# Optimization experiments

Hardware: AMD Instinct MI355X
Metric: run time of the kernel (lower is better)

Reference implementation:

```python
import jax, jax.numpy as jnp
import numpy as np

N, E, D, H = 100000, 200000, 384, 768
BN_EPS = 1e-5


def setup_inputs() -> dict:
    key = jax.random.key(0)
    ks = jax.random.split(key, 8)
    w = lambda k, sh: jax.random.normal(k, sh, jnp.float32) * 0.02
    return {
        "x": jax.random.normal(ks[0], (N, D), jnp.float32),
        "edge_attr": jax.random.normal(ks[1], (E, D), jnp.float32),
        "gamma": jnp.ones((D,), jnp.float32),
        "beta": jnp.zeros((D,), jnp.float32),
        "eps": jnp.zeros((), jnp.float32),          # GINE train_eps, init 0
        "W_edge": w(ks[2], (D, D)),
        "b_edge": jnp.zeros((D,), jnp.float32),
        "W1": w(ks[3], (D, H)),
        "b1": jnp.zeros((H,), jnp.float32),
        "W2": w(ks[4], (H, D)),
        "b2": jnp.zeros((D,), jnp.float32),
        "edge_index": jax.random.randint(ks[5], (2, E), 0, N, jnp.int32),
    }


def reference(x, edge_attr, gamma, beta, eps, W_edge, b_edge, W1, b1, W2, b2, edge_index):
    # BatchNorm1d over the node (batch) dimension, training statistics
    mu = jnp.mean(x, axis=0)
    var = jnp.var(x, axis=0)
    h = (x - mu) * jax.lax.rsqrt(var + BN_EPS) * gamma + beta  # [N, D]

    src, dst = edge_index[0], edge_index[1]  # j -> i (PyG source_to_target)
    # GINEConv message: relu(x_j + lin(edge_attr))
    msg = jax.nn.relu(h[src] + edge_attr @ W_edge + b_edge)     # [E, D]
    agg = jax.ops.segment_sum(msg, dst, num_segments=N)         # sum aggregation

    # nn((1+eps)*x_i + agg) where nn = Linear->GELU->Linear
    z = (1.0 + eps) * h + agg
    z = jax.nn.gelu(z @ W1 + b1, approximate=False) @ W2 + b2

    # residual + outer GELU activation (drop_path/dropout = identity at eval)
    return x + jax.nn.gelu(z, approximate=False)
```

## Files before the change

### kernel.cpp

```cpp
#include <hip/hip_runtime.h>
#include <hip/hip_bf16.h>

#define Df 384
#define Hf 768
#define SCAN_CH 4096

typedef __bf16 bf16x8 __attribute__((ext_vector_type(8)));
typedef float f32x4 __attribute__((ext_vector_type(4)));

struct __attribute__((aligned(4))) U12 { unsigned int x, y, z; };

__device__ inline unsigned short f2bf(float f) {
    __hip_bfloat16 h = __float2bfloat16(f);
    return __builtin_bit_cast(unsigned short, h);
}
__device__ inline float bf2f(unsigned short u) {
    unsigned int v = ((unsigned int)u) << 16;
    return __builtin_bit_cast(float, v);
}
__device__ inline float lobf(unsigned int v) { return bf2f((unsigned short)(v & 0xffff)); }
__device__ inline float hibf(unsigned int v) { return bf2f((unsigned short)(v >> 16)); }
__device__ inline unsigned int pk2(float a, float b) {
    return (unsigned int)f2bf(a) | ((unsigned int)f2bf(b) << 16);
}
__device__ inline float gelu_(float v) {
    return 0.5f * v * (1.0f + erff(v * 0.70710678118654752f));
}
__device__ inline void gload16(const void* g, void* l) {
    __builtin_amdgcn_global_load_lds(
        (const __attribute__((address_space(1))) unsigned int*)g,
        (__attribute__((address_space(3))) unsigned int*)l, 16, 0, 0);
}

__global__ void bn_stats(const float* __restrict__ x, float* __restrict__ stats, int N) {
    int t = threadIdx.x;
    int c4 = (t % 96) * 4;
    int rs = t / 96;
    float s0 = 0, s1 = 0, s2 = 0, s3 = 0, q0 = 0, q1 = 0, q2 = 0, q3 = 0;
    for (int r = blockIdx.x * 2 + rs; r < N; r += gridDim.x * 2) {
        float4 v = *(const float4*)(x + (size_t)r * Df + c4);
        s0 += v.x; s1 += v.y; s2 += v.z; s3 += v.w;
        q0 += v.x * v.x; q1 += v.y * v.y; q2 += v.z * v.z; q3 += v.w * v.w;
    }
    unsafeAtomicAdd(&stats[c4 + 0], s0);
    unsafeAtomicAdd(&stats[c4 + 1], s1);
    unsafeAtomicAdd(&stats[c4 + 2], s2);
    unsafeAtomicAdd(&stats[c4 + 3], s3);
    unsafeAtomicAdd(&stats[Df + c4 + 0], q0);
    unsafeAtomicAdd(&stats[Df + c4 + 1], q1);
    unsafeAtomicAdd(&stats[Df + c4 + 2], q2);
    unsafeAtomicAdd(&stats[Df + c4 + 3], q3);
}

__global__ void bn_finalize(const float* __restrict__ stats,
                            const float* __restrict__ gamma,
                            const float* __restrict__ beta,
                            float* __restrict__ coef, int N) {
    int c = threadIdx.x;
    float invN = 1.0f / (float)N;
    float mu = stats[c] * invN;
    float var = stats[Df + c] * invN - mu * mu;
    float rs = rsqrtf(var + 1e-5f);
    float a = gamma[c] * rs;
    coef[c] = a;
    coef[Df + c] = beta[c] - mu * a;
}

__global__ void h_kernel(const float* __restrict__ x, const float* __restrict__ coef,
                         unsigned short* __restrict__ hb, int tot8) {
    int i = blockIdx.x * 256 + threadIdx.x;
    if (i >= tot8) return;
    size_t base = (size_t)i * 8;
    int c = (int)(base % Df);
    float4 x0 = *(const float4*)(x + base);
    float4 x1 = *(const float4*)(x + base + 4);
    const float* a = coef + c;
    const float* b = coef + Df + c;
    uint4 o;
    o.x = pk2(x0.x * a[0] + b[0], x0.y * a[1] + b[1]);
    o.y = pk2(x0.z * a[2] + b[2], x0.w * a[3] + b[3]);
    o.z = pk2(x1.x * a[4] + b[4], x1.y * a[5] + b[5]);
    o.w = pk2(x1.z * a[6] + b[6], x1.w * a[7] + b[7]);
    *(uint4*)(hb + base) = o;
}

__global__ void wtrans3(const float* __restrict__ We, const float* __restrict__ W1,
                        const float* __restrict__ W2,
                        unsigned short* __restrict__ WeT, unsigned short* __restrict__ W1T,
                        unsigned short* __restrict__ W2T) {
    int idx = blockIdx.x * 256 + threadIdx.x;
    if (idx < Df * Df) {
        int k = idx / Df, n = idx % Df;
        WeT[n * Df + k] = f2bf(We[idx]);
    } else if (idx < Df * Df + Df * Hf) {
        int i = idx - Df * Df;
        int k = i / Hf, n = i % Hf;
        W1T[(size_t)n * Df + k] = f2bf(W1[i]);
    } else if (idx < Df * Df + 2 * Df * Hf) {
        int i = idx - (Df * Df + Df * Hf);
        int k = i / Df, n = i % Df;
        W2T[(size_t)n * Hf + k] = f2bf(W2[i]);
    }
}

__global__ void degree_k(const int* __restrict__ dst, int* __restrict__ deg, int E) {
    int e = blockIdx.x * 256 + threadIdx.x;
    if (e < E) atomicAdd(&deg[dst[e]], 1);
}

__global__ void scan1(const int* __restrict__ deg, int* __restrict__ off,
                      int* __restrict__ sums, int N) {
    __shared__ int ts[256];
    int t = threadIdx.x;
    int base = blockIdx.x * SCAN_CH + t * 16;
    int v[16];
    int s = 0;
    for (int j = 0; j < 16; j++) {
        int idx = base + j;
        int d = (idx < N) ? deg[idx] : 0;
        v[j] = s;
        s += d;
    }
    ts[t] = s;
    __syncthreads();
    for (int o = 1; o < 256; o <<= 1) {
        int add = (t >= o) ? ts[t - o] : 0;
        __syncthreads();
        ts[t] += add;
        __syncthreads();
    }
    int pre = t ? ts[t - 1] : 0;
    for (int j = 0; j < 16; j++) {
        int idx = base + j;
        if (idx < N) off[idx] = pre + v[j];
    }
    if (t == 255) sums[blockIdx.x] = ts[255];
}

__global__ void scan2(int* __restrict__ sums, int nb) {
    int acc = 0;
    for (int b = 0; b < nb; b++) { int v = sums[b]; sums[b] = acc; acc += v; }
    sums[nb] = acc;
}

__global__ void scan3(int* __restrict__ off, const int* __restrict__ sums, int N, int nb) {
    int idx = blockIdx.x * 256 + threadIdx.x;
    if (idx < N) off[idx] += sums[idx / SCAN_CH];
    else if (idx == N) off[N] = sums[nb];
}

__global__ void fill_k(const int* __restrict__ dst, const int* __restrict__ src,
                       int* __restrict__ cursor, int* __restrict__ srcp,
                       int* __restrict__ pose, int E) {
    int e = blockIdx.x * 256 + threadIdx.x;
    if (e >= E) return;
    int pos = atomicAdd(&cursor[dst[e]], 1);
    srcp[pos] = src[e];
    pose[e] = pos;
}

__global__ __launch_bounds__(256) void aggregate(
    const unsigned short* __restrict__ msgl, const unsigned short* __restrict__ hb,
    const int* __restrict__ off, const int* __restrict__ srcp,
    const float* __restrict__ epsp,
    unsigned short* __restrict__ zb, int N) {
    int lane = threadIdx.x & 63;
    int wid = threadIdx.x >> 6;
    int nwaves = gridDim.x * 4;
    float s1p = 1.0f + epsp[0];
    int loff = lane * 6;
    for (int i = blockIdx.x * 4 + wid; i < N; i += nwaves) {
        int o0 = off[i], o1 = off[i + 1];
        float a0 = 0, a1 = 0, a2 = 0, a3 = 0, a4 = 0, a5 = 0;
        for (int p = o0; p < o1; ++p) {
            int s = srcp[p];
            U12 mv = *(const U12*)(msgl + (size_t)p * Df + loff);
            U12 hv = *(const U12*)(hb + (size_t)s * Df + loff);
            a0 += fmaxf(lobf(mv.x) + lobf(hv.x), 0.f);
            a1 += fmaxf(hibf(mv.x) + hibf(hv.x), 0.f);
            a2 += fmaxf(lobf(mv.y) + lobf(hv.y), 0.f);
            a3 += fmaxf(hibf(mv.y) + hibf(hv.y), 0.f);
            a4 += fmaxf(lobf(mv.z) + lobf(hv.z), 0.f);
            a5 += fmaxf(hibf(mv.z) + hibf(hv.z), 0.f);
        }
        U12 hv = *(const U12*)(hb + (size_t)i * Df + loff);
        U12 o;
        o.x = pk2(s1p * lobf(hv.x) + a0, s1p * hibf(hv.x) + a1);
        o.y = pk2(s1p * lobf(hv.y) + a2, s1p * hibf(hv.y) + a3);
        o.z = pk2(s1p * lobf(hv.z) + a4, s1p * hibf(hv.z) + a5);
        *(U12*)(zb + (size_t)i * Df + loff) = o;
    }
}

__global__ __launch_bounds__(256, 3) void gemm_ts(
    const unsigned short* __restrict__ Ab,
    const unsigned short* __restrict__ Bt,
    const float* __restrict__ bias,
    unsigned short* __restrict__ outb,
    int M) {
    __shared__ __align__(16) unsigned short Bs[64 * Df];

    const int t = threadIdx.x;
    const int lane = t & 63;
    const int wid = t >> 6;
    const int fr = lane & 15;
    const int kg = lane >> 4;
    const int orig = blockIdx.x;
    const int xcd = orig & 7;
    const int local = orig >> 3;
    const int cs = local % 12;
    const int rsub = local / 12;
    const int cb = cs * 64;
    const int first = xcd * 8 + rsub;
    const int STRIPS = (M + 127) >> 7;

#pragma unroll
    for (int s = 0; s < 12; s++) {
        int u = s * 256 + t;
        int col = u / 48;
        int pos = u - col * 48;
        gload16(Bt + (size_t)(cb + col) * Df + ((pos ^ (col & 7)) << 3),
                &Bs[(s * 256 + wid * 64) * 8]);
    }
    asm volatile("s_waitcnt vmcnt(0)" ::: "memory");
    __builtin_amdgcn_s_barrier();

    float bv[4];
#pragma unroll
    for (int j = 0; j < 4; j++) bv[j] = bias[cb + j * 16 + fr];

    for (int s = first; s < STRIPS; s += 64) {
        const int r0 = s * 128 + wid * 32;
        int ra0 = r0 + fr;       if (ra0 >= M) ra0 = M - 1;
        int ra1 = r0 + 16 + fr;  if (ra1 >= M) ra1 = M - 1;
        const unsigned short* pA0 = Ab + (size_t)ra0 * Df + kg * 8;
        const unsigned short* pA1 = Ab + (size_t)ra1 * Df + kg * 8;

        f32x4 acc[2][4];
#pragma unroll
        for (int i = 0; i < 2; i++)
#pragma unroll
            for (int j = 0; j < 4; j++) acc[i][j] = (f32x4){0.f, 0.f, 0.f, 0.f};

        uint4 a0 = *(const uint4*)(pA0);
        uint4 a1 = *(const uint4*)(pA1);
#pragma unroll
        for (int kt = 0; kt < 12; kt++) {
            uint4 n0, n1;
            if (kt < 11) {
                n0 = *(const uint4*)(pA0 + (kt + 1) * 32);
                n1 = *(const uint4*)(pA1 + (kt + 1) * 32);
            } else { n0 = a0; n1 = a1; }
            bf16x8 bf[4];
#pragma unroll
            for (int j = 0; j < 4; j++) {
                const int cl = j * 16 + fr;
                const int unit = (kt * 4 + kg) ^ (cl & 7);
                bf[j] = *(const bf16x8*)&Bs[(cl * 48 + unit) * 8];
            }
            bf16x8 av0 = __builtin_bit_cast(bf16x8, a0);
            bf16x8 av1 = __builtin_bit_cast(bf16x8, a1);
#pragma unroll
            for (int j = 0; j < 4; j++) {
                acc[0][j] = __builtin_amdgcn_mfma_f32_16x16x32_bf16(av0, bf[j], acc[0][j], 0, 0, 0);
                acc[1][j] = __builtin_amdgcn_mfma_f32_16x16x32_bf16(av1, bf[j], acc[1][j], 0, 0, 0);
            }
            a0 = n0; a1 = n1;
        }

        const int kg4 = kg * 4;
#pragma unroll
        for (int i = 0; i < 2; i++) {
            const int rb = r0 + i * 16 + kg4;
#pragma unroll
            for (int r = 0; r < 4; r++) {
                const int row = rb + r;
                if (row < M) {
#pragma unroll
                    for (int j = 0; j < 4; j++) {
                        outb[(size_t)row * Hf + cb + j * 16 + fr] =
                            f2bf(gelu_(acc[i][j][r] + bv[j]));
                    }
                }
            }
        }
    }
}

template <int EPI, bool ABF16>
__global__ __launch_bounds__(256) void gemm_fused(
    const void* __restrict__ Ap, const unsigned short* __restrict__ Bt,
    const float* __restrict__ bias, int M, int K, int ncols,
    const int* __restrict__ pose,
    unsigned short* __restrict__ outb,
    const float* __restrict__ xres, float* __restrict__ outf, int ldo) {
    __shared__ __align__(16) unsigned short As[2][128 * 32];
    __shared__ __align__(16) unsigned short Bs[2][128 * 32];
    const int t = threadIdx.x;
    const int nwg = gridDim.x;
    const int orig = blockIdx.x;
    const int xcd = orig & 7;
    const int q = nwg >> 3, r = nwg & 7;
    const int wgid = (xcd < r ? xcd * (q + 1) : r * (q + 1) + (xcd - r) * q) + (orig >> 3);
    const int pp = wgid / ncols;
    const int m0 = pp * 128;
    const int n0 = (wgid - pp * ncols) * 128;

    const int lane = t & 63;
    const int wid = t >> 6;
    const int wr = (wid >> 1) << 6;
    const int wc = (wid & 1) << 6;
    const int fr = lane & 15;
    const int kg = lane >> 4;
    const int crow = lane >> 2;
    const int cseg = lane & 3;
    const int sr = t >> 1;
    const int sh = (t & 1) << 4;

    f32x4 acc[4][4];
#pragma unroll
    for (int i = 0; i < 4; i++)
#pragma unroll
        for (int j = 0; j < 4; j++) acc[i][j] = (f32x4){0.f, 0.f, 0.f, 0.f};

    const bool arok = (m0 + sr) < M;
    const size_t arowoff = (size_t)(m0 + sr) * K;
    const int NT = K >> 5;

    auto stageB = [&](int buf, int k0) {
#pragma unroll
        for (int h = 0; h < 2; h++) {
            const int rbase = wid * 32 + h * 16;
            gload16(Bt + (size_t)(n0 + rbase + crow) * K + k0 + cseg * 8,
                    &Bs[buf][rbase * 32]);
        }
    };
    auto stageA16 = [&](int buf, int k0) {
        const unsigned short* Ab = (const unsigned short*)Ap;
#pragma unroll
        for (int h = 0; h < 2; h++) {
            const int rbase = wid * 32 + h * 16;
            if (m0 + rbase + crow < M)
                gload16(Ab + (size_t)(m0 + rbase + crow) * K + k0 + cseg * 8,
                        &As[buf][rbase * 32]);
        }
    };

    if (ABF16) {
        stageA16(0, 0);
    } else if (arok) {
        const float4* p = (const float4*)((const float*)Ap + arowoff + sh);
        float4 f0 = p[0], f1 = p[1], f2 = p[2], f3 = p[3];
        uint4 w0, w1;
        w0.x = pk2(f0.x, f0.y); w0.y = pk2(f0.z, f0.w);
        w0.z = pk2(f1.x, f1.y); w0.w = pk2(f1.z, f1.w);
        w1.x = pk2(f2.x, f2.y); w1.y = pk2(f2.z, f2.w);
        w1.z = pk2(f3.x, f3.y); w1.w = pk2(f3.z, f3.w);
        *(uint4*)&As[0][sr * 32 + sh] = w0;
        *(uint4*)&As[0][sr * 32 + sh + 8] = w1;
    }
    stageB(0, 0);
    __syncthreads();

    int cur = 0;
    for (int kt = 0; kt < NT; ++kt) {
        const int nxt = cur ^ 1;
        const bool more = (kt + 1) < NT;
        float4 f0, f1, f2, f3;
        if (more) {
            const int k0n = (kt + 1) * 32;
            if (ABF16) {
                stageA16(nxt, k0n);
            } else if (arok) {
                const float4* p = (const float4*)((const float*)Ap + arowoff + k0n + sh);
                f0 = p[0]; f1 = p[1]; f2 = p[2]; f3 = p[3];
            }
            stageB(nxt, k0n);
        }

        bf16x8 a[4], b[4];
#pragma unroll
        for (int i = 0; i < 4; i++) a[i] = *(const bf16x8*)&As[cur][(wr + i * 16 + fr) * 32 + kg * 8];
#pragma unroll
        for (int j = 0; j < 4; j++) b[j] = *(const bf16x8*)&Bs[cur][(wc + j * 16 + fr) * 32 + kg * 8];
#pragma unroll
        for (int i = 0; i < 4; i++)
#pragma unroll
            for (int j = 0; j < 4; j++)
                acc[i][j] = __builtin_amdgcn_mfma_f32_16x16x32_bf16(a[i], b[j], acc[i][j], 0, 0, 0);

        if (!ABF16 && more && arok) {
            uint4 w0, w1;
            w0.x = pk2(f0.x, f0.y); w0.y = pk2(f0.z, f0.w);
            w0.z = pk2(f1.x, f1.y); w0.w = pk2(f1.z, f1.w);
            w1.x = pk2(f2.x, f2.y); w1.y = pk2(f2.z, f2.w);
            w1.z = pk2(f3.x, f3.y); w1.w = pk2(f3.z, f3.w);
            *(uint4*)&As[nxt][sr * 32 + sh] = w0;
            *(uint4*)&As[nxt][sr * 32 + sh + 8] = w1;
        }
        __syncthreads();
        cur = nxt;
    }

    const int kg4 = kg * 4;
#pragma unroll
    for (int i = 0; i < 4; i++) {
        const int rb = m0 + wr + i * 16 + kg4;
#pragma unroll
        for (int j = 0; j < 4; j++) {
            const int c = n0 + wc + j * 16 + fr;
#pragma unroll
            for (int r = 0; r < 4; r++) {
                const int row = rb + r;
                if (row < M) {
                    float v = acc[i][j][r] + bias[c];
                    if (EPI == 2) {
                        size_t o = (size_t)row * ldo + c;
                        outf[o] = xres[o] + gelu_(v);
                    } else {
                        outb[(size_t)pose[row] * ldo + c] = f2bf(v);
                    }
                }
            }
        }
    }
}

extern "C" void kernel_launch(void* const* d_in, const int* in_sizes, int n_in,
                              void* d_out, int out_size, void* d_ws, size_t ws_size,
                              hipStream_t stream) {
    const float* x = (const float*)d_in[0];
    const float* ea = (const float*)d_in[1];
    const float* gamma = (const float*)d_in[2];
    const float* beta = (const float*)d_in[3];
    const float* epsp = (const float*)d_in[4];
    const float* W_edge = (const float*)d_in[5];
    const float* b_edge = (const float*)d_in[6];
    const float* W1 = (const float*)d_in[7];
    const float* b1 = (const float*)d_in[8];
    const float* W2 = (const float*)d_in[9];
    const float* b2 = (const float*)d_in[10];
    const int* eidx = (const int*)d_in[11];
    float* out = (float*)d_out;
    const int N = in_sizes[0] / Df;
    const int E = in_sizes[1] / Df;
    const int* esrc = eidx;
    const int* edst = eidx + E;

    char* w = (char*)d_ws;
    size_t off_ = 0;
    auto alloc = [&](size_t bytes) { char* p = w + off_; off_ += (bytes + 255) & ~(size_t)255; return p; };
    float* stats = (float*)alloc(2 * Df * sizeof(float));
    float* coef = (float*)alloc(2 * Df * sizeof(float));
    unsigned short* hb = (unsigned short*)alloc((size_t)N * Df * 2);
    unsigned short* zb = (unsigned short*)alloc((size_t)N * Df * 2);
    unsigned short* tb = (unsigned short*)alloc((size_t)N * Hf * 2);
    unsigned short* WeT = (unsigned short*)alloc((size_t)Df * Df * 2);
    unsigned short* W1T = (unsigned short*)alloc((size_t)Df * Hf * 2);
    unsigned short* W2T = (unsigned short*)alloc((size_t)Hf * Df * 2);
    int* deg = (int*)alloc((size_t)(N + 1) * 4);
    int* offs = (int*)alloc((size_t)(N + 1) * 4);
    int* srcp = (int*)alloc((size_t)E * 4);
    int* pose = (int*)alloc((size_t)E * 4);
    int* sums = (int*)alloc(64 * 4);
    size_t msgl_bytes = (size_t)E * Df * 2;
    unsigned short* msgl;
    if (off_ + msgl_bytes <= ws_size) msgl = (unsigned short*)alloc(msgl_bytes);
    else msgl = (unsigned short*)d_out;
    (void)n_in; (void)out_size;

    hipMemsetAsync(stats, 0, 2 * Df * sizeof(float), stream);
    hipMemsetAsync(deg, 0, (size_t)N * 4, stream);

    bn_stats<<<1024, 192, 0, stream>>>(x, stats, N);
    bn_finalize<<<1, Df, 0, stream>>>(stats, gamma, beta, coef, N);
    int tot8 = N * Df / 8;
    h_kernel<<<(tot8 + 255) / 256, 256, 0, stream>>>(x, coef, hb, tot8);

    wtrans3<<<(Df * Df + 2 * Df * Hf + 255) / 256, 256, 0, stream>>>(
        W_edge, W1, W2, WeT, W1T, W2T);

    int nb = (N + SCAN_CH - 1) / SCAN_CH;
    degree_k<<<(E + 255) / 256, 256, 0, stream>>>(edst, deg, E);
    scan1<<<nb, 256, 0, stream>>>(deg, offs, sums, N);
    scan2<<<1, 1, 0, stream>>>(sums, nb);
    scan3<<<(N + 256) / 256, 256, 0, stream>>>(offs, sums, N, nb);
    hipMemcpyAsync(deg, offs, (size_t)N * 4, hipMemcpyDeviceToDevice, stream);
    fill_k<<<(E + 255) / 256, 256, 0, stream>>>(edst, esrc, deg, srcp, pose, E);

    int ep = (E + 127) / 128;
    gemm_fused<3, false><<<dim3(ep * (Df / 128)), 256, 0, stream>>>(
        ea, WeT, b_edge, E, Df, Df / 128, pose, msgl, nullptr, nullptr, Df);

    aggregate<<<2048, 256, 0, stream>>>(msgl, hb, offs, srcp, epsp, zb, N);

    gemm_ts<<<768, 256, 0, stream>>>(zb, W1T, b1, tb, N);

    int np = (N + 127) / 128;
    gemm_fused<2, true><<<dim3(np * (Df / 128)), 256, 0, stream>>>(
        tb, W2T, b2, N, Hf, Df / 128, nullptr, nullptr, x, out, Df);
}
```

Baseline: 1.146 ms.

## Replace persistent W1 GEMM and W2 GEMM with templated strip GEMM kernel

The persistent gemm_ts kernel is replaced by a templated one-tile-per-workgroup strip GEMM, with workgroup IDs remapped so neighbouring tiles land on the same XCD. The same kernel now also handles the second MLP GEMM (K=768), staging the B slab in two 384-wide halves, and replaces the previous gemm_fused call. The first GEMM's epilogue goes through an LDS transpose so each bf16 row is written with 16-byte stores instead of scattered 2-byte stores. The cost is reloading the B tile in every workgroup, more launched blocks, and an extra barrier in the K=768 pass.

```diff
diff --git a/kernel.cpp b/kernel.cpp
--- a/kernel.cpp
+++ b/kernel.cpp
@@ -192,62 +192,71 @@
     }
 }
 
-__global__ __launch_bounds__(256, 3) void gemm_ts(
-    const unsigned short* __restrict__ Ab,
-    const unsigned short* __restrict__ Bt,
+template <int KTOT, int EPI>
+__global__ __launch_bounds__(256, 3) void gemm_strip(
+    const unsigned short* __restrict__ Ab, const unsigned short* __restrict__ Bt,
     const float* __restrict__ bias,
-    unsigned short* __restrict__ outb,
-    int M) {
-    __shared__ __align__(16) unsigned short Bs[64 * Df];
+    unsigned short* __restrict__ outb, const float* __restrict__ xres,
+    float* __restrict__ outf, int M, int ncols, int ldo) {
+    constexpr int NKT = KTOT / 32;
+    constexpr int NH = KTOT / 384;
+    __shared__ __align__(16) unsigned short Bs[64 * 48 * 8];
 
     const int t = threadIdx.x;
+    const int nwg = gridDim.x;
+    const int orig = blockIdx.x;
+    const int xcd = orig & 7;
+    const int q = nwg >> 3, r = nwg & 7;
+    const int wgid = (xcd < r ? xcd * (q + 1) : r * (q + 1) + (xcd - r) * q) + (orig >> 3);
+    const int strip = wgid / ncols;
+    const int cb = (wgid - strip * ncols) * 64;
+
     const int lane = t & 63;
     const int wid = t >> 6;
     const int fr = lane & 15;
     const int kg = lane >> 4;
-    const int orig = blockIdx.x;
-    const int xcd = orig & 7;
-    const int local = orig >> 3;
-    const int cs = local % 12;
-    const int rsub = local / 12;
-    const int cb = cs * 64;
-    const int first = xcd * 8 + rsub;
-    const int STRIPS = (M + 127) >> 7;
-
-#pragma unroll
-    for (int s = 0; s < 12; s++) {
-        int u = s * 256 + t;
-        int col = u / 48;
-        int pos = u - col * 48;
-        gload16(Bt + (size_t)(cb + col) * Df + ((pos ^ (col & 7)) << 3),
-                &Bs[(s * 256 + wid * 64) * 8]);
-    }
+
+    auto stageB = [&](int koff) {
+#pragma unroll
+        for (int s_ = 0; s_ < 12; s_++) {
+            int u = s_ * 256 + t;
+            int col = u / 48;
+            int pos = u - col * 48;
+            gload16(Bt + (size_t)(cb + col) * KTOT + koff + ((pos ^ (col & 7)) << 3),
+                    &Bs[(s_ * 256 + wid * 64) * 8]);
+        }
+    };
+
+    int ra0 = strip * 128 + wid * 32 + fr;      if (ra0 >= M) ra0 = M - 1;
+    int ra1 = strip * 128 + wid * 32 + 16 + fr; if (ra1 >= M) ra1 = M - 1;
+    const unsigned short* pA0 = Ab + (size_t)ra0 * KTOT + kg * 8;
+    const unsigned short* pA1 = Ab + (size_t)ra1 * KTOT + kg * 8;
+
+    f32x4 acc[2][4];
+#pragma unroll
+    for (int i = 0; i < 2; i++)
+#pragma unroll
+        for (int j = 0; j < 4; j++) acc[i][j] = (f32x4){0.f, 0.f, 0.f, 0.f};
+
+    stageB(0);
+    uint4 a0 = *(const uint4*)(pA0);
+    uint4 a1 = *(const uint4*)(pA1);
     asm volatile("s_waitcnt vmcnt(0)" ::: "memory");
     __builtin_amdgcn_s_barrier();
 
-    float bv[4];
-#pragma unroll
-    for (int j = 0; j < 4; j++) bv[j] = bias[cb + j * 16 + fr];
-
-    for (int s = first; s < STRIPS; s += 64) {
-        const int r0 = s * 128 + wid * 32;
-        int ra0 = r0 + fr;       if (ra0 >= M) ra0 = M - 1;
-        int ra1 = r0 + 16 + fr;  if (ra1 >= M) ra1 = M - 1;
-        const unsigned short* pA0 = Ab + (size_t)ra0 * Df + kg * 8;
-        const unsigned short* pA1 = Ab + (size_t)ra1 * Df + kg * 8;
-
-        f32x4 acc[2][4];
-#pragma unroll
-        for (int i = 0; i < 2; i++)
-#pragma unroll
-            for (int j = 0; j < 4; j++) acc[i][j] = (f32x4){0.f, 0.f, 0.f, 0.f};
-
-        uint4 a0 = *(const uint4*)(pA0);
-        uint4 a1 = *(const uint4*)(pA1);
-#pragma unroll
-        for (int kt = 0; kt < 12; kt++) {
+#pragma unroll
+    for (int h = 0; h < NH; h++) {
+        if (h > 0) {
+            __syncthreads();
+            stageB(h * 384);
+            asm volatile("s_waitcnt vmcnt(0)" ::: "memory");
+            __builtin_amdgcn_s_barrier();
+        }
+#pragma unroll
+        for (int ktl = 0; ktl < 12; ktl++) {
+            const int kt = h * 12 + ktl;
             uint4 n0, n1;
-            if (kt < 11) {
+            if (kt < NKT - 1) {
                 n0 = *(const uint4*)(pA0 + (kt + 1) * 32);
                 n1 = *(const uint4*)(pA1 + (kt + 1) * 32);
             } else { n0 = a0; n1 = a1; }
@@ -255,7 +264,7 @@
 #pragma unroll
             for (int j = 0; j < 4; j++) {
                 const int cl = j * 16 + fr;
-                const int unit = (kt * 4 + kg) ^ (cl & 7);
+                const int unit = (ktl * 4 + kg) ^ (cl & 7);
                 bf[j] = *(const bf16x8*)&Bs[(cl * 48 + unit) * 8];
             }
             bf16x8 av0 = __builtin_bit_cast(bf16x8, a0);
@@ -267,19 +276,49 @@
             }
             a0 = n0; a1 = n1;
         }
-
-        const int kg4 = kg * 4;
+    }
+
+    float bv[4];
+#pragma unroll
+    for (int j = 0; j < 4; j++) bv[j] = bias[cb + j * 16 + fr];
+    const int kg4 = kg * 4;
+    const int rbase = strip * 128;
+
+    if (EPI == 1) {
+        __syncthreads();
+        unsigned short* Ct = Bs;
 #pragma unroll
         for (int i = 0; i < 2; i++) {
-            const int rb = r0 + i * 16 + kg4;
-#pragma unroll
-            for (int r = 0; r < 4; r++) {
-                const int row = rb + r;
+            const int rl = wid * 32 + i * 16 + kg4;
+#pragma unroll
+            for (int j = 0; j < 4; j++) {
+#pragma unroll
+                for (int rr = 0; rr < 4; rr++)
+                    Ct[(rl + rr) * 72 + j * 16 + fr] = f2bf(gelu_(acc[i][j][rr] + bv[j]));
+            }
+        }
+        __syncthreads();
+#pragma unroll
+        for (int s_ = 0; s_ < 4; s_++) {
+            int u = s_ * 256 + t;
+            int rl = u >> 3, seg = u & 7;
+            int grow = rbase + rl;
+            if (grow < M)
+                *(uint4*)(outb + (size_t)grow * ldo + cb + seg * 8) =
+                    *(const uint4*)&Ct[rl * 72 + seg * 8];
+        }
+    } else {
+#pragma unroll
+        for (int i = 0; i < 2; i++) {
+            const int rb = rbase + wid * 32 + i * 16 + kg4;
+#pragma unroll
+            for (int rr = 0; rr < 4; rr++) {
+                const int row = rb + rr;
                 if (row < M) {
 #pragma unroll
                     for (int j = 0; j < 4; j++) {
-                        outb[(size_t)row * Hf + cb + j * 16 + fr] =
-                            f2bf(gelu_(acc[i][j][r] + bv[j]));
+                        size_t o = (size_t)row * ldo + cb + j * 16 + fr;
+                        outf[o] = xres[o] + gelu_(acc[i][j][rr] + bv[j]);
                     }
                 }
             }
@@ -494,9 +533,10 @@
 
     aggregate<<<2048, 256, 0, stream>>>(msgl, hb, offs, srcp, epsp, zb, N);
 
-    gemm_ts<<<768, 256, 0, stream>>>(zb, W1T, b1, tb, N);
-
-    int np = (N + 127) / 128;
-    gemm_fused<2, true><<<dim3(np * (Df / 128)), 256, 0, stream>>>(
-        tb, W2T, b2, N, Hf, Df / 128, nullptr, nullptr, x, out, Df);
-}
+    int strips = (N + 127) / 128;
+    gemm_strip<Df, 1><<<dim3(strips * (Hf / 64)), 256, 0, stream>>>(
+        zb, W1T, b1, tb, nullptr, nullptr, N, Hf / 64, Hf);
+
+    gemm_strip<Hf, 2><<<dim3(strips * (Df / 64)), 256, 0, stream>>>(
+        tb, W2T, b2, nullptr, x, out, N, Df / 64, Df);
+}
```

Result: faster. 1.030 ms (-10.2%).
